# Performance work log

Measured on AMD Instinct MI355X. Metric: run time of the kernel, lower is better.

The kernel has to match this reference:

```python
import jax, jax.numpy as jnp
import numpy as np

NUM_EMBEDDINGS = 2048
EMBEDDING_DIM = 128
BETA = 0.25


def setup_inputs() -> dict:
    key = jax.random.key(0)
    k1, k2 = jax.random.split(key)
    z = jax.random.normal(k1, (64, 32, 32, EMBEDDING_DIM), dtype=jnp.float32)
    # nn.Embedding init: uniform(-1/K, 1/K)
    emb = jax.random.uniform(k2, (NUM_EMBEDDINGS, EMBEDDING_DIM), dtype=jnp.float32,
                             minval=-1.0 / NUM_EMBEDDINGS, maxval=1.0 / NUM_EMBEDDINGS)
    return {"z": z, "emb": emb}


def reference(z, emb):
    beta = BETA
    flat = z.reshape(-1, EMBEDDING_DIM)  # [N, D]
    dist = (jnp.sum(flat * flat, axis=1, keepdims=True)
            - 2.0 * flat @ emb.T
            + jnp.sum(emb * emb, axis=1))
    indices = jnp.argmin(dist, axis=1)  # [N]
    quantized = emb[indices].reshape(z.shape)
    # commitment / codebook loss
    loss = (jnp.mean((jax.lax.stop_gradient(quantized) - z) ** 2)
            + beta * jnp.mean((quantized - jax.lax.stop_gradient(z)) ** 2))
    # straight-through estimator
    quantized_st = z + jax.lax.stop_gradient(quantized - z)
    indices_out = indices.reshape(z.shape[0], -1)
    return quantized_st, indices_out, loss
```

## Files before the change

kernel.cpp:

```cpp
#include <hip/hip_runtime.h>

#define NUM_EMB 2048
#define DIM     128
#define NVEC    65536
#define MARGIN  1.0e-3f
#define CAP     32
#define CHUNK   512
#define NCHUNK  (NUM_EMB / CHUNK)
#define ES      136
#define ZS      132

typedef float  f32x4 __attribute__((ext_vector_type(4)));
typedef short  s16x8 __attribute__((ext_vector_type(8)));

__device__ __forceinline__ ushort f2bf(float f) {
    unsigned u = __float_as_uint(f);
    u = (u + 0x7fffu + ((u >> 16) & 1u)) >> 16;
    return (ushort)u;
}

__device__ __forceinline__ float np_pairwise_sumsq_128(const float* __restrict__ p)
{
    float r[8];
    #pragma unroll
    for (int j = 0; j < 8; ++j) { float v = p[j]; r[j] = __fmul_rn(v, v); }
    #pragma unroll
    for (int i = 8; i < 128; i += 8)
        #pragma unroll
        for (int j = 0; j < 8; ++j) { float v = p[i + j]; r[j] = __fadd_rn(r[j], __fmul_rn(v, v)); }
    float s01 = __fadd_rn(r[0], r[1]);
    float s23 = __fadd_rn(r[2], r[3]);
    float s45 = __fadd_rn(r[4], r[5]);
    float s67 = __fadd_rn(r[6], r[7]);
    return __fadd_rn(__fadd_rn(s01, s23), __fadd_rn(s45, s67));
}

__device__ __forceinline__ float dot_seg(const float4* __restrict__ zp,
                                         const float4* __restrict__ ep,
                                         int seg, float dot)
{
    float4 e[8], zz[8];
    #pragma unroll
    for (int i = 0; i < 8; ++i) { e[i] = ep[seg * 8 + i]; zz[i] = zp[seg * 8 + i]; }
    #pragma unroll
    for (int i = 0; i < 8; ++i) {
        dot = fmaf(zz[i].x, e[i].x, dot);
        dot = fmaf(zz[i].y, e[i].y, dot);
        dot = fmaf(zz[i].z, e[i].z, dot);
        dot = fmaf(zz[i].w, e[i].w, dot);
    }
    return dot;
}

__global__ __launch_bounds__(256)
void prep_kernel(const float* __restrict__ emb,
                 float* __restrict__ enorm,
                 float* __restrict__ accum,
                 ushort* __restrict__ emb_bf)
{
    int g = blockIdx.x * 256 + threadIdx.x;
    if (g == 0) *accum = 0.0f;

    float4 v = ((const float4*)emb)[g];
    ushort4 b;
    b.x = f2bf(v.x); b.y = f2bf(v.y); b.z = f2bf(v.z); b.w = f2bf(v.w);
    ((ushort4*)emb_bf)[g] = b;

    if (g < NUM_EMB)
        enorm[g] = np_pairwise_sumsq_128(emb + (size_t)g * DIM);
}

__global__ __launch_bounds__(1024, 4)
void approx_kernel(const float* __restrict__ z,
                   const ushort* __restrict__ emb_bf,
                   const float* __restrict__ enorm,
                   unsigned* __restrict__ cand_cnt,
                   ushort* __restrict__ cand)
{
    __shared__ __align__(16) ushort eS[CHUNK * ES];
    __shared__ float cS[CHUNK];
    __shared__ unsigned cntS[256];

    const int tid  = threadIdx.x;
    const int w    = tid >> 6;
    const int lane = tid & 63;
    const int col  = lane & 15;
    const int quad = lane >> 4;
    const int rowbase = blockIdx.x * 256 + w * 16;

    if (tid < 256) cntS[tid] = 0u;

    s16x8 afrag[4];
    {
        const float* zr = z + (size_t)(rowbase + col) * DIM;
        #pragma unroll
        for (int kt = 0; kt < 4; ++kt) {
            const float4* p = (const float4*)(zr + kt * 32 + quad * 8);
            float4 f0 = p[0], f1 = p[1];
            s16x8 a;
            a[0] = (short)f2bf(f0.x); a[1] = (short)f2bf(f0.y);
            a[2] = (short)f2bf(f0.z); a[3] = (short)f2bf(f0.w);
            a[4] = (short)f2bf(f1.x); a[5] = (short)f2bf(f1.y);
            a[6] = (short)f2bf(f1.z); a[7] = (short)f2bf(f1.w);
            afrag[kt] = a;
        }
    }

    float vmax[4], thr[4];
    #pragma unroll
    for (int r = 0; r < 4; ++r) { vmax[r] = -3.0e38f; thr[r] = 3.0e38f; }

    for (int vis = 0; vis < NCHUNK; ++vis) {
        if (vis > 0) __syncthreads();

        const uint4* src = (const uint4*)(emb_bf + (size_t)vis * CHUNK * DIM);
        #pragma unroll
        for (int i = 0; i < 8; ++i) {
            int li = i * 1024 + tid;
            int code = li >> 4, fc = li & 15;
            *(uint4*)&eS[code * ES + fc * 8] = src[li];
        }
        if (tid < CHUNK) cS[tid] = -0.5f * enorm[vis * CHUNK + tid];
        __syncthreads();

        #pragma unroll 4
        for (int t = 0; t < 32; ++t) {
            s16x8 bfrag[4];
            #pragma unroll
            for (int kt = 0; kt < 4; ++kt)
                bfrag[kt] = *(const s16x8*)&eS[(t * 16 + col) * ES + kt * 32 + quad * 8];

            float h = cS[t * 16 + col];
            f32x4 a = {h, h, h, h};
            #pragma unroll
            for (int kt = 0; kt < 4; ++kt)
                a = __builtin_amdgcn_mfma_f32_16x16x32_bf16(afrag[kt], bfrag[kt], a, 0, 0, 0);

            #pragma unroll
            for (int r = 0; r < 4; ++r) vmax[r] = fmaxf(vmax[r], a[r]);

            if (vis == 0) {
                #pragma unroll
                for (int r = 0; r < 4; ++r) {
                    float v = vmax[r];
                    v = fmaxf(v, __shfl_xor(v, 1, 64));
                    v = fmaxf(v, __shfl_xor(v, 2, 64));
                    v = fmaxf(v, __shfl_xor(v, 4, 64));
                    v = fmaxf(v, __shfl_xor(v, 8, 64));
                    vmax[r] = v;
                    thr[r]  = v - 0.5f * MARGIN;
                }
            }

            const int code_g = vis * CHUNK + t * 16 + col;
            #pragma unroll
            for (int r = 0; r < 4; ++r) {
                if (a[r] >= thr[r]) {
                    int row_l = w * 16 + quad * 4 + r;
                    unsigned pos = atomicAdd(&cntS[row_l], 1u);
                    if (pos < CAP)
                        cand[(size_t)(blockIdx.x * 256 + row_l) * CAP + pos] = (ushort)code_g;
                }
            }
        }

        if (vis > 0) {
            #pragma unroll
            for (int r = 0; r < 4; ++r) {
                float v = vmax[r];
                v = fmaxf(v, __shfl_xor(v, 1, 64));
                v = fmaxf(v, __shfl_xor(v, 2, 64));
                v = fmaxf(v, __shfl_xor(v, 4, 64));
                v = fmaxf(v, __shfl_xor(v, 8, 64));
                vmax[r] = v;
                thr[r]  = v - 0.5f * MARGIN;
            }
        }
    }

    __syncthreads();
    if (tid < 256) cand_cnt[blockIdx.x * 256 + tid] = cntS[tid];
}

__global__ __launch_bounds__(256)
void rerank_kernel(const float* __restrict__ z,
                   const float* __restrict__ emb,
                   const float* __restrict__ enorm,
                   const unsigned* __restrict__ cand_cnt,
                   const ushort* __restrict__ cand,
                   float* __restrict__ out_q,
                   float* __restrict__ out_idx_f,
                   float* __restrict__ accum)
{
    __shared__ float zs[64 * ZS];
    __shared__ float As[64];
    __shared__ int   bidx[64];
    __shared__ int   ovf_list[64];
    __shared__ int   ovf_n;
    __shared__ float rv[4];
    __shared__ int   rvi[4];
    __shared__ float wsum[4];

    const int tid = threadIdx.x;
    const int m0  = blockIdx.x * 64;
    if (tid == 0) ovf_n = 0;

    #pragma unroll
    for (int i = 0; i < 8; ++i) {
        int li = tid + i * 256;
        int m  = li >> 5, dc = li & 31;
        float4 v = ((const float4*)(z + (size_t)(m0 + m) * DIM))[dc];
        *(float4*)&zs[m * ZS + dc * 4] = v;
    }
    __syncthreads();
    if (tid < 64) As[tid] = np_pairwise_sumsq_128(&zs[tid * ZS]);
    __syncthreads();

    const int row_l = tid >> 2;
    const int sub   = tid & 3;
    const int row_g = m0 + row_l;
    const unsigned cnt = cand_cnt[row_g];
    const float A = As[row_l];
    const float4* zp = (const float4*)&zs[row_l * ZS];

    float bv = 3.0e38f;
    int   bi = 0x7fffffff;

    if (cnt <= CAP) {
        for (unsigned ci = sub; ci < cnt; ci += 4) {
            int j = (int)cand[(size_t)row_g * CAP + ci];
            const float4* ep = (const float4*)(emb + (size_t)j * DIM);
            float dot = 0.0f;
            #pragma unroll
            for (int seg = 0; seg < 4; ++seg) dot = dot_seg(zp, ep, seg, dot);
            float t1 = fmaf(-2.0f, dot, A);
            float s  = __fadd_rn(t1, enorm[j]);
            if (s < bv || (s == bv && j < bi)) { bv = s; bi = j; }
        }
    }
    #pragma unroll
    for (int off = 1; off <= 2; off <<= 1) {
        float v  = __shfl_xor(bv, off, 64);
        int   ix = __shfl_xor(bi, off, 64);
        if (v < bv || (v == bv && ix < bi)) { bv = v; bi = ix; }
    }
    if (sub == 0) {
        if (cnt <= CAP) bidx[row_l] = bi;
        else { int p = atomicAdd(&ovf_n, 1); ovf_list[p] = row_l; }
    }
    __syncthreads();

    const int n_ovf = ovf_n;
    for (int o = 0; o < n_ovf; ++o) {
        const int rl = ovf_list[o];
        const float Ar = As[rl];
        const float4* zp2 = (const float4*)&zs[rl * ZS];
        float bv2 = 3.0e38f;
        int   bi2 = 0x7fffffff;
        for (int jj = 0; jj < 8; ++jj) {
            int j = tid * 8 + jj;
            const float4* ep = (const float4*)(emb + (size_t)j * DIM);
            float dot = 0.0f;
            #pragma unroll
            for (int seg = 0; seg < 4; ++seg) dot = dot_seg(zp2, ep, seg, dot);
            float t1 = fmaf(-2.0f, dot, Ar);
            float s  = __fadd_rn(t1, enorm[j]);
            if (s < bv2) { bv2 = s; bi2 = j; }
        }
        #pragma unroll
        for (int off = 1; off < 64; off <<= 1) {
            float v  = __shfl_xor(bv2, off, 64);
            int   ix = __shfl_xor(bi2, off, 64);
            if (v < bv2 || (v == bv2 && ix < bi2)) { bv2 = v; bi2 = ix; }
        }
        if ((tid & 63) == 0) { rv[tid >> 6] = bv2; rvi[tid >> 6] = bi2; }
        __syncthreads();
        if (tid == 0) {
            float fv = rv[0]; int fi = rvi[0];
            #pragma unroll
            for (int ww = 1; ww < 4; ++ww) {
                if (rv[ww] < fv || (rv[ww] == fv && rvi[ww] < fi)) { fv = rv[ww]; fi = rvi[ww]; }
            }
            bidx[rl] = fi;
        }
        __syncthreads();
    }

    if (tid < 64) out_idx_f[m0 + tid] = (float)bidx[tid];

    float part = 0.0f;
    #pragma unroll
    for (int i = 0; i < 8; ++i) {
        int li = tid + i * 256;
        int m  = li >> 5, dc = li & 31;
        int j  = bidx[m];
        float4 q  = ((const float4*)(emb + (size_t)j * DIM))[dc];
        float4 zv = *(const float4*)&zs[m * ZS + dc * 4];
        float4 o;
        o.x = __fadd_rn(zv.x, __fsub_rn(q.x, zv.x));
        o.y = __fadd_rn(zv.y, __fsub_rn(q.y, zv.y));
        o.z = __fadd_rn(zv.z, __fsub_rn(q.z, zv.z));
        o.w = __fadd_rn(zv.w, __fsub_rn(q.w, zv.w));
        ((float4*)out_q)[(size_t)(m0 + m) * 32 + dc] = o;
        float dx = q.x - zv.x, dy = q.y - zv.y, dz = q.z - zv.z, dw = q.w - zv.w;
        part += dx * dx + dy * dy + dz * dz + dw * dw;
    }
    #pragma unroll
    for (int off = 32; off > 0; off >>= 1)
        part += __shfl_down(part, off, 64);
    if ((tid & 63) == 0) wsum[tid >> 6] = part;
    __syncthreads();
    if (tid == 0) atomicAdd(accum, wsum[0] + wsum[1] + wsum[2] + wsum[3]);
}

__global__ void finalize_kernel(const float* __restrict__ accum,
                                float* __restrict__ out_loss)
{
    *out_loss = 1.25f * (*accum) / 8388608.0f;
}

extern "C" void kernel_launch(void* const* d_in, const int* in_sizes, int n_in,
                              void* d_out, int out_size, void* d_ws, size_t ws_size,
                              hipStream_t stream)
{
    const float* z   = (const float*)d_in[0];
    const float* emb = (const float*)d_in[1];
    float* out = (float*)d_out;

    char*     ws       = (char*)d_ws;
    float*    enorm    = (float*)ws;
    float*    accum    = (float*)(ws + 8192);
    unsigned* cand_cnt = (unsigned*)(ws + 16384);
    ushort*   cand     = (ushort*)(ws + 16384 + 262144);
    ushort*   emb_bf   = (ushort*)(ws + 16384 + 262144 + 4194304);

    prep_kernel   <<<NVEC / 256, 256,  0, stream>>>(emb, enorm, accum, emb_bf);
    approx_kernel <<<NVEC / 256, 1024, 0, stream>>>(z, emb_bf, enorm, cand_cnt, cand);
    rerank_kernel <<<NVEC / 64,  256,  0, stream>>>(z, emb, enorm, cand_cnt, cand,
                                                    out, out + 8388608, accum);
    finalize_kernel<<<1, 1, 0, stream>>>(accum, out + 8388608 + 65536);
}
```

Before: 242.0 us.

## Tile approx kernel as 32 rows per wave pair sharing B fragments

Each wave now handles 32 rows (two M-tiles) against half of each 512-code chunk, so every B fragment loaded from LDS feeds two MFMAs. This halves the LDS reads of the codebook per MFMA. Running maxima are exchanged between the paired waves through a small shared array at each chunk boundary to keep the pruning thresholds consistent. In exchange it adds register pressure from the doubled A fragments and accumulators, and the thresholds are slightly staler within a chunk.

```diff
diff --git a/kernel.cpp b/kernel.cpp
--- a/kernel.cpp
+++ b/kernel.cpp
@@ -79,6 +79,7 @@
 {
     __shared__ __align__(16) ushort eS[CHUNK * ES];
     __shared__ float cS[CHUNK];
+    __shared__ float vS[16][32];
     __shared__ unsigned cntS[256];
 
     const int tid  = threadIdx.x;
@@ -86,13 +87,16 @@
     const int lane = tid & 63;
     const int col  = lane & 15;
     const int quad = lane >> 4;
-    const int rowbase = blockIdx.x * 256 + w * 16;
+    const int rg   = w >> 1;
+    const int ch   = w & 1;
+    const int rowbase = blockIdx.x * 256 + rg * 32;
 
     if (tid < 256) cntS[tid] = 0u;
 
-    s16x8 afrag[4];
-    {
-        const float* zr = z + (size_t)(rowbase + col) * DIM;
+    s16x8 afrag[2][4];
+    #pragma unroll
+    for (int mt = 0; mt < 2; ++mt) {
+        const float* zr = z + (size_t)(rowbase + mt * 16 + col) * DIM;
         #pragma unroll
         for (int kt = 0; kt < 4; ++kt) {
             const float4* p = (const float4*)(zr + kt * 32 + quad * 8);
@@ -102,13 +106,16 @@
             a[2] = (short)f2bf(f0.z); a[3] = (short)f2bf(f0.w);
             a[4] = (short)f2bf(f1.x); a[5] = (short)f2bf(f1.y);
             a[6] = (short)f2bf(f1.z); a[7] = (short)f2bf(f1.w);
-            afrag[kt] = a;
-        }
-    }
-
-    float vmax[4], thr[4];
-    #pragma unroll
-    for (int r = 0; r < 4; ++r) { vmax[r] = -3.0e38f; thr[r] = 3.0e38f; }
+            afrag[mt][kt] = a;
+        }
+    }
+
+    const ushort* eH = eS + ch * 256 * ES;
+    const float*  cH = cS + ch * 256;
+
+    float vmax[8], thr[8];
+    #pragma unroll
+    for (int i = 0; i < 8; ++i) { vmax[i] = -3.0e38f; thr[i] = 3.0e38f; }
 
     for (int vis = 0; vis < NCHUNK; ++vis) {
         if (vis > 0) __syncthreads();
@@ -121,60 +128,86 @@
             *(uint4*)&eS[code * ES + fc * 8] = src[li];
         }
         if (tid < CHUNK) cS[tid] = -0.5f * enorm[vis * CHUNK + tid];
+
+        if (vis > 0) {
+            #pragma unroll
+            for (int i = 0; i < 8; ++i) {
+                float v = fmaxf(vmax[i], vS[w ^ 1][(i >> 2) * 16 + quad * 4 + (i & 3)]);
+                vmax[i] = v;
+                thr[i]  = v - 0.5f * MARGIN;
+            }
+        }
         __syncthreads();
 
         #pragma unroll 4
-        for (int t = 0; t < 32; ++t) {
+        for (int t = 0; t < 16; ++t) {
             s16x8 bfrag[4];
             #pragma unroll
             for (int kt = 0; kt < 4; ++kt)
-                bfrag[kt] = *(const s16x8*)&eS[(t * 16 + col) * ES + kt * 32 + quad * 8];
-
-            float h = cS[t * 16 + col];
-            f32x4 a = {h, h, h, h};
-            #pragma unroll
-            for (int kt = 0; kt < 4; ++kt)
-                a = __builtin_amdgcn_mfma_f32_16x16x32_bf16(afrag[kt], bfrag[kt], a, 0, 0, 0);
-
-            #pragma unroll
-            for (int r = 0; r < 4; ++r) vmax[r] = fmaxf(vmax[r], a[r]);
+                bfrag[kt] = *(const s16x8*)&eH[(t * 16 + col) * ES + kt * 32 + quad * 8];
+
+            float h = cH[t * 16 + col];
+            f32x4 a0 = {h, h, h, h};
+            f32x4 a1 = {h, h, h, h};
+            #pragma unroll
+            for (int kt = 0; kt < 4; ++kt) {
+                a0 = __builtin_amdgcn_mfma_f32_16x16x32_bf16(afrag[0][kt], bfrag[kt], a0, 0, 0, 0);
+                a1 = __builtin_amdgcn_mfma_f32_16x16x32_bf16(afrag[1][kt], bfrag[kt], a1, 0, 0, 0);
+            }
+
+            #pragma unroll
+            for (int r = 0; r < 4; ++r) {
+                vmax[r]     = fmaxf(vmax[r],     a0[r]);
+                vmax[4 + r] = fmaxf(vmax[4 + r], a1[r]);
+            }
 
             if (vis == 0) {
                 #pragma unroll
-                for (int r = 0; r < 4; ++r) {
-                    float v = vmax[r];
+                for (int i = 0; i < 8; ++i) {
+                    float v = vmax[i];
                     v = fmaxf(v, __shfl_xor(v, 1, 64));
                     v = fmaxf(v, __shfl_xor(v, 2, 64));
                     v = fmaxf(v, __shfl_xor(v, 4, 64));
                     v = fmaxf(v, __shfl_xor(v, 8, 64));
-                    vmax[r] = v;
-                    thr[r]  = v - 0.5f * MARGIN;
+                    vmax[i] = v;
+                    thr[i]  = v - 0.5f * MARGIN;
                 }
             }
 
-            const int code_g = vis * CHUNK + t * 16 + col;
+            const int code_g = vis * CHUNK + ch * 256 + t * 16 + col;
             #pragma unroll
             for (int r = 0; r < 4; ++r) {
-                if (a[r] >= thr[r]) {
-                    int row_l = w * 16 + quad * 4 + r;
+                if (a0[r] >= thr[r]) {
+                    int row_l = rg * 32 + quad * 4 + r;
                     unsigned pos = atomicAdd(&cntS[row_l], 1u);
                     if (pos < CAP)
                         cand[(size_t)(blockIdx.x * 256 + row_l) * CAP + pos] = (ushort)code_g;
                 }
+                if (a1[r] >= thr[4 + r]) {
+                    int row_l = rg * 32 + 16 + quad * 4 + r;
+                    unsigned pos = atomicAdd(&cntS[row_l], 1u);
+                    if (pos < CAP)
+                        cand[(size_t)(blockIdx.x * 256 + row_l) * CAP + pos] = (ushort)code_g;
+                }
             }
         }
 
         if (vis > 0) {
             #pragma unroll
-            for (int r = 0; r < 4; ++r) {
-                float v = vmax[r];
+            for (int i = 0; i < 8; ++i) {
+                float v = vmax[i];
                 v = fmaxf(v, __shfl_xor(v, 1, 64));
                 v = fmaxf(v, __shfl_xor(v, 2, 64));
                 v = fmaxf(v, __shfl_xor(v, 4, 64));
                 v = fmaxf(v, __shfl_xor(v, 8, 64));
-                vmax[r] = v;
-                thr[r]  = v - 0.5f * MARGIN;
-            }
+                vmax[i] = v;
+                thr[i]  = v - 0.5f * MARGIN;
+            }
+        }
+        if (col == 0) {
+            #pragma unroll
+            for (int i = 0; i < 8; ++i)
+                vS[w][(i >> 2) * 16 + quad * 4 + (i & 3)] = vmax[i];
         }
     }
 
```

Result: slower. 259.4 us (+7.2%).
